# Kernel tuning notes

Hardware: AMD Instinct MI355X
Metric: run time of the kernel (lower is better)

Reference implementation:

```python
import jax, jax.numpy as jnp
import numpy as np

WIDTH = 1024
NUM_HEADS = 16
HEAD_DIM = WIDTH // NUM_HEADS  # 64
WINDOW = 256
BATCH = 2
SEQ = 2048
_MIN_LOGITS_VALUE = -1e30


def setup_inputs() -> dict:
    key = jax.random.key(0)
    ks = jax.random.split(key, 6)
    std = 1.0 / np.sqrt(WIDTH)
    x = jax.random.normal(ks[0], (BATCH, SEQ, WIDTH), dtype=jnp.float32)
    Wq = jax.random.normal(ks[1], (WIDTH, WIDTH), dtype=jnp.float32) * std
    Wk = jax.random.normal(ks[2], (HEAD_DIM, WIDTH), dtype=jnp.float32) * std
    Wv = jax.random.normal(ks[3], (HEAD_DIM, WIDTH), dtype=jnp.float32) * std
    Wf = jax.random.normal(ks[4], (WIDTH, WIDTH), dtype=jnp.float32) * std  # variance_scale=1.0
    bf = jnp.zeros((WIDTH,), dtype=jnp.float32)
    return {"x": x, "Wq": Wq, "Wk": Wk, "Wv": Wv, "Wf": Wf, "bf": bf}


def reference(x, Wq, Wk, Wv, Wf, bf):
    b, t, _ = x.shape
    # projections (torch Linear: y = x @ W.T)
    q = (x @ Wq.T).reshape(b, t, NUM_HEADS, HEAD_DIM)  # b t n h
    k = x @ Wk.T  # b t h  (MQA: single shared key head)
    v = x @ Wv.T  # b t h
    scale = 1.0 / np.sqrt(HEAD_DIM)
    # logits: queries per-head against the shared key head
    logits = jnp.einsum('btnh,bsh->bnts', q, k) * scale  # b n t s
    # symmetric local window mask |i - j| <= WINDOW
    pos = jnp.arange(t)
    mask = jnp.abs(pos[:, None] - pos[None, :]) <= WINDOW  # t s
    masked = jnp.where(mask[None, None, :, :], logits, _MIN_LOGITS_VALUE)
    probs = jax.nn.softmax(masked.astype(jnp.float32), axis=-1).astype(logits.dtype)
    out = jnp.einsum('bnts,bsh->btnh', probs, v).reshape(b, t, WIDTH)
    return out @ Wf.T + bf
```

## Files before the change

### kernel.cpp

```cpp
#include <hip/hip_runtime.h>

typedef __bf16 bf16;
typedef __bf16 bf16x8 __attribute__((ext_vector_type(8)));
typedef float  f32x4  __attribute__((ext_vector_type(4)));

#define MFMA(a, b, c) __builtin_amdgcn_mfma_f32_16x16x32_bf16((a), (b), (c), 0, 0, 0)

static constexpr int B_   = 2;
static constexpr int T_   = 2048;
static constexpr int D_   = 1024;
static constexpr int NH_  = 16;
static constexpr int HD_  = 64;
static constexpr int WIN_ = 256;
static constexpr int M_   = B_ * T_;
static constexpr int NQKV = D_ + 2 * HD_;

__device__ __forceinline__ void gld_lds16(const bf16* g, bf16* l) {
  __builtin_amdgcn_global_load_lds(
      (const __attribute__((address_space(1))) void*)g,
      (__attribute__((address_space(3))) void*)l, 16, 0, 0);
}

__global__ __launch_bounds__(256) void conv_all(
    const float* __restrict__ x,  const float* __restrict__ wq,
    const float* __restrict__ wk, const float* __restrict__ wv,
    const float* __restrict__ wf, const float* __restrict__ bv,
    bf16* __restrict__ xc, bf16* __restrict__ wqkv,
    bf16* __restrict__ wfc, bf16* __restrict__ bfc) {
  const long i = (long)(blockIdx.x * 256 + threadIdx.x) * 4;
  const float* src; bf16* dst; long off;
  if      (i < 4194304L) { src = x;  dst = xc;              off = 0; }
  else if (i < 5242880L) { src = wq; dst = wqkv;            off = 4194304L; }
  else if (i < 5308416L) { src = wk; dst = wqkv + 1048576L; off = 5242880L; }
  else if (i < 5373952L) { src = wv; dst = wqkv + 1114112L; off = 5308416L; }
  else if (i < 6422528L) { src = wf; dst = wfc;             off = 5373952L; }
  else if (i < 6423552L) { src = bv; dst = bfc;             off = 6422528L; }
  else return;
  const long j = i - off;
  const float4 v = *(const float4*)(src + j);
  bf16 o[4] = {(bf16)v.x, (bf16)v.y, (bf16)v.z, (bf16)v.w};
  *(uint2*)(dst + j) = *(const uint2*)o;
}

template <int EPI>
__global__ __launch_bounds__(256) void gemm64x128(
    const bf16* __restrict__ A, const bf16* __restrict__ Bw,
    void* __restrict__ Cout, const bf16* __restrict__ bias,
    bf16* __restrict__ kb, bf16* __restrict__ vT, int N, int K) {
  __shared__ __align__(16) bf16 As[64 * 64];
  __shared__ __align__(16) bf16 Bs[128 * 64];

  const int tid  = threadIdx.x;
  const int w    = tid >> 6;
  const int lane = tid & 63;
  const int quad = lane >> 4;
  const int l16  = lane & 15;
  const int wm   = w & 1;
  const int wn   = w >> 1;
  const int m0   = blockIdx.x * 64;
  const int n0   = blockIdx.y * 128;
  const int lrow = lane >> 3;
  const int lcol = (lane & 7) * 8;

  f32x4 acc[2][4] = {};

  for (int k0 = 0; k0 < K; k0 += 64) {
    __syncthreads();
#pragma unroll
    for (int t = 0; t < 6; ++t) {
      const int inst = w * 6 + t;
      if (inst < 8) {
        gld_lds16(&A[(size_t)(m0 + inst * 8 + lrow) * K + k0 + lcol],
                  &As[inst * 512]);
      } else {
        const int bi = inst - 8;
        gld_lds16(&Bw[(size_t)(n0 + bi * 8 + lrow) * K + k0 + lcol],
                  &Bs[bi * 512]);
      }
    }
    __syncthreads();
#pragma unroll
    for (int kk = 0; kk < 64; kk += 32) {
      bf16x8 a[2], b[4];
#pragma unroll
      for (int i = 0; i < 2; ++i)
        a[i] = *(const bf16x8*)&As[(wm * 32 + i * 16 + l16) * 64 + kk + quad * 8];
#pragma unroll
      for (int j = 0; j < 4; ++j)
        b[j] = *(const bf16x8*)&Bs[(wn * 64 + j * 16 + l16) * 64 + kk + quad * 8];
#pragma unroll
      for (int i = 0; i < 2; ++i)
#pragma unroll
        for (int j = 0; j < 4; ++j) acc[i][j] = MFMA(a[i], b[j], acc[i][j]);
    }
  }

#pragma unroll
  for (int i = 0; i < 2; ++i) {
#pragma unroll
    for (int j = 0; j < 4; ++j) {
      const int col     = n0 + wn * 64 + j * 16 + l16;
      const int rowbase = m0 + wm * 32 + i * 16 + quad * 4;
      if (EPI == 1) {
        if (col < D_) {
          bf16* qb = (bf16*)Cout;
#pragma unroll
          for (int r = 0; r < 4; ++r)
            qb[(size_t)(rowbase + r) * D_ + col] = (bf16)(acc[i][j][r] * 0.125f);
        } else if (col < D_ + HD_) {
#pragma unroll
          for (int r = 0; r < 4; ++r)
            kb[(size_t)(rowbase + r) * HD_ + (col - D_)] = (bf16)acc[i][j][r];
        } else {
          bf16 o[4] = {(bf16)acc[i][j][0], (bf16)acc[i][j][1],
                       (bf16)acc[i][j][2], (bf16)acc[i][j][3]};
          *(uint2*)&vT[(size_t)(col - D_ - HD_) * M_ + rowbase] = *(const uint2*)o;
        }
      } else {
        float* outp = (float*)Cout;
        const float bvv = (float)bias[col];
#pragma unroll
        for (int r = 0; r < 4; ++r)
          outp[(size_t)(rowbase + r) * D_ + col] = acc[i][j][r] + bvv;
      }
    }
  }
}

__global__ __launch_bounds__(256) void attn_win128(
    const bf16* __restrict__ q, const bf16* __restrict__ k,
    const bf16* __restrict__ vT, bf16* __restrict__ o) {
  __shared__ __align__(16) bf16 Qs[128 * 64];
  __shared__ __align__(16) bf16 Ks[2][64 * 64];
  __shared__ __align__(16) bf16 Vt[2][64 * 64];
  __shared__ __align__(16) bf16 Ps[128 * 72];
  __shared__ float ls[4][32];

  const int tid  = threadIdx.x;
  const int w    = tid >> 6;
  const int lane = tid & 63;
  const int quad = lane >> 4;
  const int l16  = lane & 15;
  const int lrow = lane >> 3;
  const int lcol = (lane & 7) * 8;

  const int t0 = blockIdx.x * 128;
  const int n  = blockIdx.y;
  const int b  = blockIdx.z;

#pragma unroll
  for (int t = 0; t < 4; ++t) {
    const int inst = w * 4 + t;
    gld_lds16(&q[((size_t)(b * T_ + t0 + inst * 8 + lrow)) * D_ + n * HD_ + lcol],
              &Qs[inst * 512]);
  }

  auto stageKV = [&](int st, int pb) {
#pragma unroll
    for (int t = 0; t < 2; ++t) {
      const int inst = w * 2 + t;
      gld_lds16(&k[((size_t)(b * T_ + st + inst * 8 + lrow)) * HD_ + lcol],
                &Ks[pb][inst * 512]);
      gld_lds16(&vT[(size_t)(inst * 8 + lrow) * M_ + b * T_ + st + lcol],
                &Vt[pb][inst * 512]);
    }
  };

  const int st_lo = (t0 - WIN_ > 0) ? t0 - WIN_ : 0;
  const int st_hi = (t0 + WIN_ + 64 < T_ - 64) ? t0 + WIN_ + 64 : T_ - 64;

  stageKV(st_lo, 0);
  int pb = 0;

  f32x4 o_acc[2][4] = {};
  float l_part[2] = {0.0f, 0.0f};

  for (int st = st_lo; st <= st_hi; st += 64) {
    __syncthreads();
    if (st + 64 <= st_hi) stageKV(st + 64, pb ^ 1);

    f32x4 sacc[4][2] = {};
#pragma unroll
    for (int kk = 0; kk < 64; kk += 32) {
      bf16x8 ak[4], bq[2];
#pragma unroll
      for (int stile = 0; stile < 4; ++stile)
        ak[stile] = *(const bf16x8*)&Ks[pb][(stile * 16 + l16) * 64 + kk + quad * 8];
#pragma unroll
      for (int tt = 0; tt < 2; ++tt)
        bq[tt] = *(const bf16x8*)&Qs[(w * 32 + tt * 16 + l16) * 64 + kk + quad * 8];
#pragma unroll
      for (int stile = 0; stile < 4; ++stile)
#pragma unroll
        for (int tt = 0; tt < 2; ++tt)
          sacc[stile][tt] = MFMA(ak[stile], bq[tt], sacc[stile][tt]);
    }

    const int off_t = st - t0;
    const bool need_mask =
        (off_t < w * 32 - (WIN_ - 31)) || (off_t > w * 32 + (WIN_ - 63));
    if (!need_mask) {
#pragma unroll
      for (int tt = 0; tt < 2; ++tt) {
#pragma unroll
        for (int stile = 0; stile < 4; ++stile) {
          bf16 pk[4];
          float psum = 0.0f;
#pragma unroll
          for (int r = 0; r < 4; ++r) {
            const float p = __expf(fminf(sacc[stile][tt][r], 30.0f));
            psum += p;
            pk[r] = (bf16)p;
          }
          l_part[tt] += psum;
          *(uint2*)&Ps[(w * 32 + tt * 16 + l16) * 72 + stile * 16 + quad * 4] =
              *(const uint2*)pk;
        }
      }
    } else {
#pragma unroll
      for (int tt = 0; tt < 2; ++tt) {
        const int t = t0 + w * 32 + tt * 16 + l16;
#pragma unroll
        for (int stile = 0; stile < 4; ++stile) {
          bf16 pk[4];
          float psum = 0.0f;
#pragma unroll
          for (int r = 0; r < 4; ++r) {
            const int s = st + stile * 16 + quad * 4 + r;
            const int d = t - s;
            const float p = (d > WIN_ || d < -WIN_)
                                ? 0.0f
                                : __expf(fminf(sacc[stile][tt][r], 30.0f));
            psum += p;
            pk[r] = (bf16)p;
          }
          l_part[tt] += psum;
          *(uint2*)&Ps[(w * 32 + tt * 16 + l16) * 72 + stile * 16 + quad * 4] =
              *(const uint2*)pk;
        }
      }
    }
    __syncthreads();

#pragma unroll
    for (int kk = 0; kk < 64; kk += 32) {
      bf16x8 ap[2];
#pragma unroll
      for (int rg = 0; rg < 2; ++rg)
        ap[rg] = *(const bf16x8*)&Ps[(w * 32 + rg * 16 + l16) * 72 + kk + quad * 8];
#pragma unroll
      for (int nt = 0; nt < 4; ++nt) {
        bf16x8 bv = *(const bf16x8*)&Vt[pb][(nt * 16 + l16) * 64 + kk + quad * 8];
#pragma unroll
        for (int rg = 0; rg < 2; ++rg)
          o_acc[rg][nt] = MFMA(ap[rg], bv, o_acc[rg][nt]);
      }
    }
    pb ^= 1;
  }

#pragma unroll
  for (int tt = 0; tt < 2; ++tt) {
    l_part[tt] += __shfl_xor(l_part[tt], 16);
    l_part[tt] += __shfl_xor(l_part[tt], 32);
    if (quad == 0) ls[w][tt * 16 + l16] = l_part[tt];
  }
  __syncthreads();

#pragma unroll
  for (int rg = 0; rg < 2; ++rg) {
#pragma unroll
    for (int r = 0; r < 4; ++r) {
      const float lr = ls[w][rg * 16 + quad * 4 + r] + 1e-30f;
      const int t = t0 + w * 32 + rg * 16 + quad * 4 + r;
#pragma unroll
      for (int nt = 0; nt < 4; ++nt) {
        const int h = nt * 16 + l16;
        o[((size_t)(b * T_ + t)) * D_ + n * HD_ + h] =
            (bf16)(o_acc[rg][nt][r] / lr);
      }
    }
  }
}

extern "C" void kernel_launch(void* const* d_in, const int* in_sizes, int n_in,
                              void* d_out, int out_size, void* d_ws, size_t ws_size,
                              hipStream_t stream) {
  float* out = (float*)d_out;

  bf16* xc   = (bf16*)d_ws;
  bf16* wqkv = xc   + (size_t)M_ * D_;
  bf16* wfc  = wqkv + (size_t)NQKV * D_;
  bf16* bfc  = wfc  + (size_t)D_ * D_;
  bf16* qb   = bfc  + D_;
  bf16* kb   = qb   + (size_t)M_ * D_;
  bf16* vT   = kb   + (size_t)M_ * HD_;

  dim3 blk(256);
  conv_all<<<dim3((6423552 / 4 + 255) / 256), blk, 0, stream>>>(
      (const float*)d_in[0], (const float*)d_in[1], (const float*)d_in[2],
      (const float*)d_in[3], (const float*)d_in[4], (const float*)d_in[5],
      xc, wqkv, wfc, bfc);

  gemm64x128<1><<<dim3(M_ / 64, NQKV / 128), blk, 0, stream>>>(
      xc, wqkv, (void*)qb, nullptr, kb, vT, NQKV, D_);

  attn_win128<<<dim3(T_ / 128, NH_, B_), blk, 0, stream>>>(qb, kb, vT, qb);

  gemm64x128<2><<<dim3(M_ / 64, D_ / 128), blk, 0, stream>>>(
      qb, wfc, (void*)out, bfc, nullptr, nullptr, D_, D_);
}
```

Measured before the change: 156.5 us.

## Use two waves per attention block with 64 query rows each and register-held Q

The attention kernel now runs with 128 threads (two waves) instead of four. Each wave handles 64 query rows and keeps its Q fragments in registers across the whole KV loop instead of reloading them from LDS every tile. The PV product is transposed so each lane ends up holding a full row's denominator, which removes the LDS reduction of row sums and lets each lane write four contiguous bf16 outputs. The cost is fewer waves per block and more accumulator registers per wave, which may reduce latency hiding.

```diff
diff --git a/kernel.cpp b/kernel.cpp
--- a/kernel.cpp
+++ b/kernel.cpp
@@ -127,14 +127,13 @@
   }
 }
 
-__global__ __launch_bounds__(256) void attn_win128(
+__global__ __launch_bounds__(128, 1) void attn_win128(
     const bf16* __restrict__ q, const bf16* __restrict__ k,
     const bf16* __restrict__ vT, bf16* __restrict__ o) {
   __shared__ __align__(16) bf16 Qs[128 * 64];
   __shared__ __align__(16) bf16 Ks[2][64 * 64];
   __shared__ __align__(16) bf16 Vt[2][64 * 64];
   __shared__ __align__(16) bf16 Ps[128 * 72];
-  __shared__ float ls[4][32];
 
   const int tid  = threadIdx.x;
   const int w    = tid >> 6;
@@ -149,16 +148,16 @@
   const int b  = blockIdx.z;
 
 #pragma unroll
-  for (int t = 0; t < 4; ++t) {
-    const int inst = w * 4 + t;
+  for (int t = 0; t < 8; ++t) {
+    const int inst = w * 8 + t;
     gld_lds16(&q[((size_t)(b * T_ + t0 + inst * 8 + lrow)) * D_ + n * HD_ + lcol],
               &Qs[inst * 512]);
   }
 
   auto stageKV = [&](int st, int pb) {
 #pragma unroll
-    for (int t = 0; t < 2; ++t) {
-      const int inst = w * 2 + t;
+    for (int t = 0; t < 4; ++t) {
+      const int inst = w * 4 + t;
       gld_lds16(&k[((size_t)(b * T_ + st + inst * 8 + lrow)) * HD_ + lcol],
                 &Ks[pb][inst * 512]);
       gld_lds16(&vT[(size_t)(inst * 8 + lrow) * M_ + b * T_ + st + lcol],
@@ -170,38 +169,44 @@
   const int st_hi = (t0 + WIN_ + 64 < T_ - 64) ? t0 + WIN_ + 64 : T_ - 64;
 
   stageKV(st_lo, 0);
+  __syncthreads();
+
+  bf16x8 bq[4][2];
+#pragma unroll
+  for (int tt = 0; tt < 4; ++tt)
+#pragma unroll
+    for (int kc = 0; kc < 2; ++kc)
+      bq[tt][kc] =
+          *(const bf16x8*)&Qs[(w * 64 + tt * 16 + l16) * 64 + kc * 32 + quad * 8];
+
   int pb = 0;
-
-  f32x4 o_acc[2][4] = {};
-  float l_part[2] = {0.0f, 0.0f};
+  f32x4 o_acc[4][4] = {};
+  float l_part[4] = {};
 
   for (int st = st_lo; st <= st_hi; st += 64) {
-    __syncthreads();
     if (st + 64 <= st_hi) stageKV(st + 64, pb ^ 1);
 
-    f32x4 sacc[4][2] = {};
-#pragma unroll
-    for (int kk = 0; kk < 64; kk += 32) {
-      bf16x8 ak[4], bq[2];
+    f32x4 sacc[4][4] = {};
+#pragma unroll
+    for (int kc = 0; kc < 2; ++kc) {
+      bf16x8 ak[4];
 #pragma unroll
       for (int stile = 0; stile < 4; ++stile)
-        ak[stile] = *(const bf16x8*)&Ks[pb][(stile * 16 + l16) * 64 + kk + quad * 8];
-#pragma unroll
-      for (int tt = 0; tt < 2; ++tt)
-        bq[tt] = *(const bf16x8*)&Qs[(w * 32 + tt * 16 + l16) * 64 + kk + quad * 8];
+        ak[stile] =
+            *(const bf16x8*)&Ks[pb][(stile * 16 + l16) * 64 + kc * 32 + quad * 8];
 #pragma unroll
       for (int stile = 0; stile < 4; ++stile)
 #pragma unroll
-        for (int tt = 0; tt < 2; ++tt)
-          sacc[stile][tt] = MFMA(ak[stile], bq[tt], sacc[stile][tt]);
+        for (int tt = 0; tt < 4; ++tt)
+          sacc[stile][tt] = MFMA(ak[stile], bq[tt][kc], sacc[stile][tt]);
     }
 
     const int off_t = st - t0;
     const bool need_mask =
-        (off_t < w * 32 - (WIN_ - 31)) || (off_t > w * 32 + (WIN_ - 63));
+        (off_t < w * 64 - 193) || (off_t > w * 64 + 193);
     if (!need_mask) {
 #pragma unroll
-      for (int tt = 0; tt < 2; ++tt) {
+      for (int tt = 0; tt < 4; ++tt) {
 #pragma unroll
         for (int stile = 0; stile < 4; ++stile) {
           bf16 pk[4];
@@ -213,14 +218,14 @@
             pk[r] = (bf16)p;
           }
           l_part[tt] += psum;
-          *(uint2*)&Ps[(w * 32 + tt * 16 + l16) * 72 + stile * 16 + quad * 4] =
+          *(uint2*)&Ps[(w * 64 + tt * 16 + l16) * 72 + stile * 16 + quad * 4] =
               *(const uint2*)pk;
         }
       }
     } else {
 #pragma unroll
-      for (int tt = 0; tt < 2; ++tt) {
-        const int t = t0 + w * 32 + tt * 16 + l16;
+      for (int tt = 0; tt < 4; ++tt) {
+        const int t = t0 + w * 64 + tt * 16 + l16;
 #pragma unroll
         for (int stile = 0; stile < 4; ++stile) {
           bf16 pk[4];
@@ -236,7 +241,7 @@
             pk[r] = (bf16)p;
           }
           l_part[tt] += psum;
-          *(uint2*)&Ps[(w * 32 + tt * 16 + l16) * 72 + stile * 16 + quad * 4] =
+          *(uint2*)&Ps[(w * 64 + tt * 16 + l16) * 72 + stile * 16 + quad * 4] =
               *(const uint2*)pk;
         }
       }
@@ -244,42 +249,43 @@
     __syncthreads();
 
 #pragma unroll
-    for (int kk = 0; kk < 64; kk += 32) {
-      bf16x8 ap[2];
-#pragma unroll
-      for (int rg = 0; rg < 2; ++rg)
-        ap[rg] = *(const bf16x8*)&Ps[(w * 32 + rg * 16 + l16) * 72 + kk + quad * 8];
-#pragma unroll
-      for (int nt = 0; nt < 4; ++nt) {
-        bf16x8 bv = *(const bf16x8*)&Vt[pb][(nt * 16 + l16) * 64 + kk + quad * 8];
-#pragma unroll
-        for (int rg = 0; rg < 2; ++rg)
-          o_acc[rg][nt] = MFMA(ap[rg], bv, o_acc[rg][nt]);
-      }
-    }
+    for (int kc = 0; kc < 2; ++kc) {
+      bf16x8 ap[4], bv[4];
+#pragma unroll
+      for (int tt = 0; tt < 4; ++tt)
+        ap[tt] =
+            *(const bf16x8*)&Ps[(w * 64 + tt * 16 + l16) * 72 + kc * 32 + quad * 8];
+#pragma unroll
+      for (int nt = 0; nt < 4; ++nt)
+        bv[nt] =
+            *(const bf16x8*)&Vt[pb][(nt * 16 + l16) * 64 + kc * 32 + quad * 8];
+#pragma unroll
+      for (int nt = 0; nt < 4; ++nt)
+#pragma unroll
+        for (int tt = 0; tt < 4; ++tt)
+          o_acc[nt][tt] = MFMA(bv[nt], ap[tt], o_acc[nt][tt]);
+    }
+    __syncthreads();
     pb ^= 1;
   }
 
 #pragma unroll
-  for (int tt = 0; tt < 2; ++tt) {
+  for (int tt = 0; tt < 4; ++tt) {
     l_part[tt] += __shfl_xor(l_part[tt], 16);
     l_part[tt] += __shfl_xor(l_part[tt], 32);
-    if (quad == 0) ls[w][tt * 16 + l16] = l_part[tt];
-  }
-  __syncthreads();
-
-#pragma unroll
-  for (int rg = 0; rg < 2; ++rg) {
-#pragma unroll
-    for (int r = 0; r < 4; ++r) {
-      const float lr = ls[w][rg * 16 + quad * 4 + r] + 1e-30f;
-      const int t = t0 + w * 32 + rg * 16 + quad * 4 + r;
-#pragma unroll
-      for (int nt = 0; nt < 4; ++nt) {
-        const int h = nt * 16 + l16;
-        o[((size_t)(b * T_ + t)) * D_ + n * HD_ + h] =
-            (bf16)(o_acc[rg][nt][r] / lr);
-      }
+  }
+
+#pragma unroll
+  for (int tt = 0; tt < 4; ++tt) {
+    const float lr = l_part[tt] + 1e-30f;
+    const int t = t0 + w * 64 + tt * 16 + l16;
+#pragma unroll
+    for (int nt = 0; nt < 4; ++nt) {
+      bf16 ov[4];
+#pragma unroll
+      for (int r = 0; r < 4; ++r) ov[r] = (bf16)(o_acc[nt][tt][r] / lr);
+      *(uint2*)&o[((size_t)(b * T_ + t)) * D_ + n * HD_ + nt * 16 + quad * 4] =
+          *(const uint2*)ov;
     }
   }
 }
@@ -306,7 +312,7 @@
   gemm64x128<1><<<dim3(M_ / 64, NQKV / 128), blk, 0, stream>>>(
       xc, wqkv, (void*)qb, nullptr, kb, vT, NQKV, D_);
 
-  attn_win128<<<dim3(T_ / 128, NH_, B_), blk, 0, stream>>>(qb, kb, vT, qb);
+  attn_win128<<<dim3(T_ / 128, NH_, B_), dim3(128), 0, stream>>>(qb, kb, vT, qb);
 
   gemm64x128<2><<<dim3(M_ / 64, D_ / 128), blk, 0, stream>>>(
       qb, wfc, (void*)out, bfc, nullptr, nullptr, D_, D_);
```

Result: no change. 156.7 us (+0.2%).

## Hoist Q fragments to registers and transpose PV MFMA for vectorized output

Applied to the files above, without the earlier changes.

Q fragments are loaded from LDS once into registers before the KV loop instead of being reloaded on every tile. The PV MFMA operands are swapped so each lane holds output values along the head dimension. This allows the row-sum normalizer to stay in registers, which removes the LDS staging and its barrier, and lets each lane write 4 bf16 outputs as one packed store. The loop barrier moves to the end of each iteration, and the extra Q registers add register pressure.

```diff
diff --git a/kernel.cpp b/kernel.cpp
--- a/kernel.cpp
+++ b/kernel.cpp
@@ -134,7 +134,6 @@
   __shared__ __align__(16) bf16 Ks[2][64 * 64];
   __shared__ __align__(16) bf16 Vt[2][64 * 64];
   __shared__ __align__(16) bf16 Ps[128 * 72];
-  __shared__ float ls[4][32];
 
   const int tid  = threadIdx.x;
   const int w    = tid >> 6;
@@ -170,30 +169,36 @@
   const int st_hi = (t0 + WIN_ + 64 < T_ - 64) ? t0 + WIN_ + 64 : T_ - 64;
 
   stageKV(st_lo, 0);
+  __syncthreads();
+
+  bf16x8 bq[2][2];
+#pragma unroll
+  for (int tt = 0; tt < 2; ++tt)
+#pragma unroll
+    for (int kc = 0; kc < 2; ++kc)
+      bq[tt][kc] =
+          *(const bf16x8*)&Qs[(w * 32 + tt * 16 + l16) * 64 + kc * 32 + quad * 8];
+
   int pb = 0;
-
   f32x4 o_acc[2][4] = {};
-  float l_part[2] = {0.0f, 0.0f};
+  float l_part[2] = {};
 
   for (int st = st_lo; st <= st_hi; st += 64) {
-    __syncthreads();
     if (st + 64 <= st_hi) stageKV(st + 64, pb ^ 1);
 
     f32x4 sacc[4][2] = {};
 #pragma unroll
-    for (int kk = 0; kk < 64; kk += 32) {
-      bf16x8 ak[4], bq[2];
+    for (int kc = 0; kc < 2; ++kc) {
+      bf16x8 ak[4];
 #pragma unroll
       for (int stile = 0; stile < 4; ++stile)
-        ak[stile] = *(const bf16x8*)&Ks[pb][(stile * 16 + l16) * 64 + kk + quad * 8];
-#pragma unroll
-      for (int tt = 0; tt < 2; ++tt)
-        bq[tt] = *(const bf16x8*)&Qs[(w * 32 + tt * 16 + l16) * 64 + kk + quad * 8];
+        ak[stile] =
+            *(const bf16x8*)&Ks[pb][(stile * 16 + l16) * 64 + kc * 32 + quad * 8];
 #pragma unroll
       for (int stile = 0; stile < 4; ++stile)
 #pragma unroll
         for (int tt = 0; tt < 2; ++tt)
-          sacc[stile][tt] = MFMA(ak[stile], bq[tt], sacc[stile][tt]);
+          sacc[stile][tt] = MFMA(ak[stile], bq[tt][kc], sacc[stile][tt]);
     }
 
     const int off_t = st - t0;
@@ -244,19 +249,23 @@
     __syncthreads();
 
 #pragma unroll
-    for (int kk = 0; kk < 64; kk += 32) {
-      bf16x8 ap[2];
+    for (int kc = 0; kc < 2; ++kc) {
+      bf16x8 ap[2], bv[4];
 #pragma unroll
       for (int rg = 0; rg < 2; ++rg)
-        ap[rg] = *(const bf16x8*)&Ps[(w * 32 + rg * 16 + l16) * 72 + kk + quad * 8];
-#pragma unroll
-      for (int nt = 0; nt < 4; ++nt) {
-        bf16x8 bv = *(const bf16x8*)&Vt[pb][(nt * 16 + l16) * 64 + kk + quad * 8];
-#pragma unroll
-        for (int rg = 0; rg < 2; ++rg)
-          o_acc[rg][nt] = MFMA(ap[rg], bv, o_acc[rg][nt]);
-      }
-    }
+        ap[rg] =
+            *(const bf16x8*)&Ps[(w * 32 + rg * 16 + l16) * 72 + kc * 32 + quad * 8];
+#pragma unroll
+      for (int nt = 0; nt < 4; ++nt)
+        bv[nt] =
+            *(const bf16x8*)&Vt[pb][(nt * 16 + l16) * 64 + kc * 32 + quad * 8];
+#pragma unroll
+      for (int rg = 0; rg < 2; ++rg)
+#pragma unroll
+        for (int nt = 0; nt < 4; ++nt)
+          o_acc[rg][nt] = MFMA(bv[nt], ap[rg], o_acc[rg][nt]);
+    }
+    __syncthreads();
     pb ^= 1;
   }
 
@@ -264,22 +273,19 @@
   for (int tt = 0; tt < 2; ++tt) {
     l_part[tt] += __shfl_xor(l_part[tt], 16);
     l_part[tt] += __shfl_xor(l_part[tt], 32);
-    if (quad == 0) ls[w][tt * 16 + l16] = l_part[tt];
-  }
-  __syncthreads();
+  }
 
 #pragma unroll
   for (int rg = 0; rg < 2; ++rg) {
-#pragma unroll
-    for (int r = 0; r < 4; ++r) {
-      const float lr = ls[w][rg * 16 + quad * 4 + r] + 1e-30f;
-      const int t = t0 + w * 32 + rg * 16 + quad * 4 + r;
-#pragma unroll
-      for (int nt = 0; nt < 4; ++nt) {
-        const int h = nt * 16 + l16;
-        o[((size_t)(b * T_ + t)) * D_ + n * HD_ + h] =
-            (bf16)(o_acc[rg][nt][r] / lr);
-      }
+    const float lr = l_part[rg] + 1e-30f;
+    const int t = t0 + w * 32 + rg * 16 + l16;
+#pragma unroll
+    for (int nt = 0; nt < 4; ++nt) {
+      bf16 ov[4];
+#pragma unroll
+      for (int r = 0; r < 4; ++r) ov[r] = (bf16)(o_acc[rg][nt][r] / lr);
+      *(uint2*)&o[((size_t)(b * T_ + t)) * D_ + n * HD_ + nt * 16 + quad * 4] =
+          *(const uint2*)ov;
     }
   }
 }
```

After: 156.7 us. About the same (+0.2%).
